# Optimization experiments

Hardware: AMD Instinct MI355X
Metric: run time of the kernel (lower is better)

Reference implementation:

```python
import jax, jax.numpy as jnp
import numpy as np
import math

B, S, D, H = 16, 1024, 768, 12
Dh = D // H  # 64


def setup_inputs() -> dict:
    key = jax.random.key(0)
    ks = jax.random.split(key, 9)
    scale = 1.0 / math.sqrt(D)
    X = jax.random.normal(ks[0], (B, S, D), dtype=jnp.float32)
    # Per-head Q/K/V projections stacked along head dim: [H, D, Dh]
    Wq = jax.random.normal(ks[1], (H, D, Dh), dtype=jnp.float32) * scale
    Wk = jax.random.normal(ks[2], (H, D, Dh), dtype=jnp.float32) * scale
    Wv = jax.random.normal(ks[3], (H, D, Dh), dtype=jnp.float32) * scale
    bq = jax.random.normal(ks[4], (H, Dh), dtype=jnp.float32) * scale
    bk = jax.random.normal(ks[5], (H, Dh), dtype=jnp.float32) * scale
    bv = jax.random.normal(ks[6], (H, Dh), dtype=jnp.float32) * scale
    Wo = jax.random.normal(ks[7], (D, D), dtype=jnp.float32) * scale
    bo = jax.random.normal(ks[8], (D,), dtype=jnp.float32) * scale
    return {"X": X, "Wq": Wq, "bq": bq, "Wk": Wk, "bk": bk,
            "Wv": Wv, "bv": bv, "Wo": Wo, "bo": bo}


def reference(X, Wq, bq, Wk, bk, Wv, bv, Wo, bo):
    # Batched multi-head QKV projections (equivalent to the per-head Linear loop).
    Q = jnp.einsum('bsd,hde->bhse', X, Wq) + bq[None, :, None, :]
    K = jnp.einsum('bsd,hde->bhse', X, Wk) + bk[None, :, None, :]
    V = jnp.einsum('bsd,hde->bhse', X, Wv) + bv[None, :, None, :]
    scores = jnp.einsum('bhse,bhte->bhst', Q, K) / jnp.sqrt(jnp.float32(Dh))
    A = jax.nn.softmax(scores, axis=-1)            # [B,H,S,S]
    O = jnp.einsum('bhst,bhte->bhse', A, V)        # [B,H,S,Dh]
    # Concat heads along feature dim (matches torch cat order: head 0 first).
    msa = jnp.transpose(O, (0, 2, 1, 3)).reshape(B, S, D)
    return msa @ Wo + bo
```

## Files before the change

### kernel.cpp

```cpp
#include <hip/hip_runtime.h>
#include <hip/hip_bf16.h>

#define BB 16
#define SS 1024
#define DD 768
#define HH 12
#define DH 64

typedef short short8 __attribute__((ext_vector_type(8)));
typedef float f32x4 __attribute__((ext_vector_type(4)));

__device__ inline float b2f(unsigned short v) {
    union { unsigned int u; float f; } x; x.u = ((unsigned int)v) << 16; return x.f;
}
__device__ inline unsigned short f2b(float f) {
    unsigned int u = __float_as_uint(f);
    u += 0x7FFFu + ((u >> 16) & 1u);
    return (unsigned short)(u >> 16);
}
__device__ inline unsigned int pk2(float a, float b) {
    __hip_bfloat162 h = __float22bfloat162_rn(make_float2(a, b));
    return *(unsigned int*)&h;
}
__device__ __forceinline__ float fast_exp2(float x) {
#if __has_builtin(__builtin_amdgcn_exp2f)
    return __builtin_amdgcn_exp2f(x);
#else
    return exp2f(x);
#endif
}
__device__ inline void cvt8(unsigned short* dst, const float* src) {
    const float4 f0 = *(const float4*)src;
    const float4 f1 = *(const float4*)(src + 4);
    unsigned short t[8] = {f2b(f0.x), f2b(f0.y), f2b(f0.z), f2b(f0.w),
                           f2b(f1.x), f2b(f1.y), f2b(f1.z), f2b(f1.w)};
    *(uint4*)dst = *(const uint4*)t;
}
__device__ __forceinline__ void async16(const void* g, void* l) {
    __builtin_amdgcn_global_load_lds(
        (const __attribute__((address_space(1))) void*)g,
        (__attribute__((address_space(3))) void*)l, 16, 0, 0);
}

__global__ __launch_bounds__(256) void detect_kernel(const unsigned short* __restrict__ X,
                                                     int* __restrict__ flag) {
    __shared__ int s;
    if (threadIdx.x == 0) s = 0;
    __syncthreads();
    int c = 0;
    for (int i = threadIdx.x; i < 16384; i += 256) {
        unsigned short v = X[i];
        if ((v & 0x7FFFu) >= 0x7F80u) c = 1;
    }
    if (c) s = 1;
    __syncthreads();
    if (threadIdx.x == 0) flag[0] = s;
}

__global__ __launch_bounds__(256) void prep_all(
    const void* __restrict__ Xv,
    const void* __restrict__ Wqv, const void* __restrict__ bqv,
    const void* __restrict__ Wkv, const void* __restrict__ bkv,
    const void* __restrict__ Wvv, const void* __restrict__ bvv,
    const void* __restrict__ Wov, const void* __restrict__ bov,
    const int* __restrict__ flag,
    unsigned short* __restrict__ Xb, unsigned short* __restrict__ Wc,
    unsigned short* __restrict__ Wot, unsigned short* __restrict__ bc,
    float* __restrict__ bo32)
{
    __shared__ unsigned short Ls[64][72];
    const int dt = *flag;
    const int u = threadIdx.x;
    const int bx = blockIdx.x;

    if (bx < 6144) {
        size_t base = ((size_t)bx * 256 + u) * 8;
        if (dt) cvt8(Xb + base, (const float*)Xv + base);
        else    *(uint4*)(Xb + base) = *(const uint4*)((const unsigned short*)Xv + base);
        return;
    }
    if (bx < 6720) {
        const int idx = bx - 6144;
        const int kt = idx % 12;
        const int y  = idx / 12;
        const int rk = u >> 2;
        const int e0 = (u & 3) * 16;

        const void* src; size_t srcBase;
        unsigned short* dst; int drow;
        if (y < 36) {
            int z = y / 12, h = y % 12;
            src = (z == 0) ? Wqv : (z == 1) ? Wkv : Wvv;
            srcBase = ((size_t)h * DD + kt * 64 + rk) * DH;
            dst = Wc; drow = z * 768 + h * 64;
        } else {
            int nt = y - 36;
            src = Wov;
            srcBase = (size_t)(kt * 64 + rk) * DD + nt * 64;
            dst = Wot; drow = nt * 64;
        }
#pragma unroll
        for (int ii = 0; ii < 2; ++ii) {
            int e = e0 + ii * 8;
            if (dt) {
                const float* p = (const float*)src + srcBase + e;
                float4 a = *(const float4*)p, b = *(const float4*)(p + 4);
                float v[8] = {a.x, a.y, a.z, a.w, b.x, b.y, b.z, b.w};
#pragma unroll
                for (int j = 0; j < 8; ++j) Ls[e + j][rk] = f2b(v[j]);
            } else {
                union { uint4 v; unsigned short s[8]; } t;
                t.v = *(const uint4*)((const unsigned short*)src + srcBase + e);
#pragma unroll
                for (int j = 0; j < 8; ++j) Ls[e + j][rk] = t.s[j];
            }
        }
        __syncthreads();
        const int e = u >> 2, q = u & 3;
#pragma unroll
        for (int ii = 0; ii < 2; ++ii) {
            int kk = q * 16 + ii * 8;
            *(uint4*)(dst + (size_t)(drow + e) * DD + kt * 64 + kk) = *(const uint4*)(&Ls[e][kk]);
        }
        return;
    }
    for (int n = u; n < 2304; n += 256) {
        int z = n / 768, i = n % 768;
        const void* b = (z == 0) ? bqv : (z == 1) ? bkv : bvv;
        bc[n] = dt ? f2b(((const float*)b)[i]) : ((const unsigned short*)b)[i];
    }
    for (int n = u; n < 768; n += 256)
        bo32[n] = dt ? ((const float*)bov)[n] : b2f(((const unsigned short*)bov)[n]);
}

__global__ __launch_bounds__(256) void qkv_gemm(
    const unsigned short* __restrict__ Xb,
    const unsigned short* __restrict__ Wc,
    const unsigned short* __restrict__ bc,
    unsigned short* __restrict__ Qb, unsigned short* __restrict__ Kb,
    unsigned short* __restrict__ Vtb)
{
    __shared__ __align__(16) unsigned short lds[17408];
    unsigned short* As = lds;
    unsigned short* Bs = lds + 128 * 64;

    const int u = threadIdx.x;
    const int lane = u & 63, w = u >> 6;
    const int ln = lane & 15, quad = lane >> 4;
    const int wm = w & 1, wn = w >> 1;

    const int nt0 = blockIdx.x;
    const int m0  = blockIdx.y << 7;
    const int n0  = nt0 << 7;
    const int z   = nt0 / 6;
    const int hpair = (nt0 % 6) * 2;

    const int rA = w * 32 + (lane >> 3);
    const int c8 = (((lane & 7) ^ (lane >> 3)) * 8);

    f32x4 acc[4][4];
#pragma unroll
    for (int i = 0; i < 4; ++i)
#pragma unroll
        for (int j = 0; j < 4; ++j) acc[i][j] = (f32x4){0.f, 0.f, 0.f, 0.f};

    const unsigned short* Ag = Xb + (size_t)(m0 + rA) * DD + c8;
    const unsigned short* Bg = Wc + (size_t)(n0 + rA) * DD + c8;
    unsigned short* lA0 = As + w * 2048;
    unsigned short* lB0 = Bs + w * 2048;

    for (int kb = 0; kb < 12; ++kb) {
        const int k0 = kb * 64;
        if (kb) __syncthreads();
#pragma unroll
        for (int j = 0; j < 4; ++j) {
            async16(Ag + (size_t)j * 8 * DD + k0, lA0 + j * 512);
            async16(Bg + (size_t)j * 8 * DD + k0, lB0 + j * 512);
        }
        __syncthreads();
#pragma unroll
        for (int kh = 0; kh < 2; ++kh) {
            const int sx = ((kh * 4 + quad) ^ (ln & 7)) * 8;
            short8 af[4], bf[4];
#pragma unroll
            for (int t = 0; t < 4; ++t) {
                af[t] = *(const short8*)(As + (wm * 64 + t * 16 + ln) * 64 + sx);
                bf[t] = *(const short8*)(Bs + (wn * 64 + t * 16 + ln) * 64 + sx);
            }
#pragma unroll
            for (int mt = 0; mt < 4; ++mt)
#pragma unroll
                for (int nt = 0; nt < 4; ++nt)
                    acc[mt][nt] = __builtin_amdgcn_mfma_f32_16x16x32_bf16(af[mt], bf[nt], acc[mt][nt], 0, 0, 0);
        }
    }

    float bias[4];
#pragma unroll
    for (int nt = 0; nt < 4; ++nt) bias[nt] = b2f(bc[n0 + wn * 64 + nt * 16 + ln]);

    const int b = m0 >> 10;
    if (z < 2) {
        unsigned short* O = (z == 0) ? Qb : Kb;
        const float sc = (z == 0) ? 0.180336880111120f : 1.0f;
        const int h = hpair + wn;
        const int sb = (m0 & 1023) + wm * 64;
#pragma unroll
        for (int mt = 0; mt < 4; ++mt)
#pragma unroll
            for (int r = 0; r < 4; ++r) {
                int s = sb + mt * 16 + quad * 4 + r;
                size_t rowo = ((size_t)(b * HH + h) * SS + s) * DH;
#pragma unroll
                for (int nt = 0; nt < 4; ++nt)
                    O[rowo + nt * 16 + ln] = f2b((acc[mt][nt][r] + bias[nt]) * sc);
            }
    } else {
        __syncthreads();
#pragma unroll
        for (int mt = 0; mt < 4; ++mt)
#pragma unroll
            for (int nt = 0; nt < 4; ++nt)
#pragma unroll
                for (int r = 0; r < 4; ++r)
                    lds[(wn * 64 + nt * 16 + ln) * 136 + wm * 64 + mt * 16 + quad * 4 + r] =
                        f2b(acc[mt][nt][r] + bias[nt]);
        __syncthreads();
        const int cc = u >> 1, half = u & 1;
        const int h = hpair + (cc >> 6), e = cc & 63;
        const int sb = (m0 & 1023) + half * 64;
        unsigned short* dst = Vtb + ((size_t)(b * HH + h) * DH + e) * SS + sb;
        const unsigned short* srcp = lds + cc * 136 + half * 64;
#pragma unroll
        for (int i = 0; i < 8; ++i)
            *(uint4*)(dst + i * 8) = *(const uint4*)(srcp + i * 8);
    }
}

__global__ __launch_bounds__(256, 3) void attn_kernel(
    const unsigned short* __restrict__ Kb,
    const unsigned short* __restrict__ Vtb,
    unsigned short* __restrict__ Qb)
{
    __shared__ __align__(16) unsigned short QPs[8192];
    __shared__ __align__(16) unsigned short Ks[2][4096];
    __shared__ __align__(16) unsigned short Vs[2][4096];

    const int u = threadIdx.x;
    const int flat = (blockIdx.y << 3) | blockIdx.x;
    const int swz  = (flat & 7) * 192 + (flat >> 3);
    const int s0 = (swz & 7) << 7;
    const int bh = swz >> 3;

    const int lane = u & 63, w = u >> 6;
    const int ln = lane & 15, quad = lane >> 4;

    unsigned short* Qg = Qb + ((size_t)bh * SS + s0) * DH;
    const unsigned short* Kg = Kb + (size_t)bh * SS * DH;
    const unsigned short* Vg = Vtb + (size_t)bh * DH * SS;

    const int srow = lane >> 3;
    const int cg8  = ((lane & 7) ^ srow) * 8;

    const unsigned short* kp0 = Kg + (size_t)((w * 2 + 0) * 8 + srow) * DH + cg8;
    const unsigned short* kp1 = Kg + (size_t)((w * 2 + 1) * 8 + srow) * DH + cg8;
    const unsigned short* vp0 = Vg + (size_t)((w * 2 + 0) * 8 + srow) * SS + cg8;
    const unsigned short* vp1 = Vg + (size_t)((w * 2 + 1) * 8 + srow) * SS + cg8;

#pragma unroll
    for (int j = 0; j < 4; ++j) {
        const int r0 = (w * 4 + j) * 8 + srow;
        async16(Qg + (size_t)r0 * DH + cg8, QPs + (w * 4 + j) * 512);
    }
    async16(kp0, &Ks[0][(w * 2 + 0) * 512]);
    async16(kp1, &Ks[0][(w * 2 + 1) * 512]);
    async16(vp0, &Vs[0][(w * 2 + 0) * 512]);
    async16(vp1, &Vs[0][(w * 2 + 1) * 512]);
    kp0 += 64 * DH; kp1 += 64 * DH; vp0 += 64; vp1 += 64;
    __syncthreads();

    short8 qf[2][2];
#pragma unroll
    for (int b = 0; b < 2; ++b) {
        const int rb = b * 64 + 16 * w + ln;
#pragma unroll
        for (int kh = 0; kh < 2; ++kh)
            qf[b][kh] = *(const short8*)(QPs + rb * 64 + ((kh * 4 + quad) ^ (ln & 7)) * 8);
    }

    short8 ones;
#pragma unroll
    for (int i = 0; i < 8; ++i) ones[i] = (short)0x3F80;

    f32x4 acc_o[2][4];
#pragma unroll
    for (int b = 0; b < 2; ++b)
#pragma unroll
        for (int i = 0; i < 4; ++i) acc_o[b][i] = (f32x4){0.f, 0.f, 0.f, 0.f};
    f32x4 acc_l[2];
    acc_l[0] = (f32x4){0.f, 0.f, 0.f, 0.f};
    acc_l[1] = (f32x4){0.f, 0.f, 0.f, 0.f};

    const unsigned short* kb0 = &Ks[0][0] + ln * 64 + ((quad ^ (ln & 7)) * 8);
    const unsigned short* kb1 = &Ks[0][0] + ln * 64 + (((4 + quad) ^ (ln & 7)) * 8);
    const unsigned short* vb0 = &Vs[0][0] + ln * 64 + ((quad ^ (ln & 7)) * 8);
    const unsigned short* vb1 = &Vs[0][0] + ln * 64 + (((4 + quad) ^ (ln & 7)) * 8);

    for (int kt = 0; kt < 16; ++kt) {
        const int cur = kt & 1;
        if (kt < 15) {
            unsigned short* lk = &Ks[cur ^ 1][(w * 2) * 512];
            unsigned short* lv = &Vs[cur ^ 1][(w * 2) * 512];
            async16(kp0, lk);
            async16(kp1, lk + 512);
            async16(vp0, lv);
            async16(vp1, lv + 512);
            kp0 += 64 * DH; kp1 += 64 * DH; vp0 += 64; vp1 += 64;
        }
        const int cb = cur * 4096;

        f32x4 acc_s[2][4];
#pragma unroll
        for (int nt = 0; nt < 4; ++nt) {
            short8 kf0 = *(const short8*)(kb0 + cb + nt * 1024);
            short8 kf1 = *(const short8*)(kb1 + cb + nt * 1024);
#pragma unroll
            for (int b = 0; b < 2; ++b) {
                f32x4 zz = (f32x4){0.f, 0.f, 0.f, 0.f};
                zz = __builtin_amdgcn_mfma_f32_16x16x32_bf16(kf0, qf[b][0], zz, 0, 0, 0);
                zz = __builtin_amdgcn_mfma_f32_16x16x32_bf16(kf1, qf[b][1], zz, 0, 0, 0);
                acc_s[b][nt] = zz;
            }
        }

#pragma unroll
        for (int b = 0; b < 2; ++b) {
            unsigned short* pb = QPs + (b * 64 + 16 * w + ln) * 64 + (quad & 1) * 4;
#pragma unroll
            for (int nt = 0; nt < 4; ++nt) {
                uint2 pw;
                pw.x = pk2(fast_exp2(acc_s[b][nt][0]), fast_exp2(acc_s[b][nt][1]));
                pw.y = pk2(fast_exp2(acc_s[b][nt][2]), fast_exp2(acc_s[b][nt][3]));
                const int c = (nt * 2 + (quad >> 1)) ^ (ln & 7);
                *(uint2*)(pb + c * 8) = pw;
            }
        }

        short8 pf[2][2];
#pragma unroll
        for (int b = 0; b < 2; ++b) {
            const unsigned short* pr = QPs + (b * 64 + 16 * w + ln) * 64;
            pf[b][0] = *(const short8*)(pr + ((quad ^ (ln & 7)) * 8));
            pf[b][1] = *(const short8*)(pr + (((4 + quad) ^ (ln & 7)) * 8));
            acc_l[b] = __builtin_amdgcn_mfma_f32_16x16x32_bf16(pf[b][0], ones, acc_l[b], 0, 0, 0);
            acc_l[b] = __builtin_amdgcn_mfma_f32_16x16x32_bf16(pf[b][1], ones, acc_l[b], 0, 0, 0);
        }
#pragma unroll
        for (int nt = 0; nt < 4; ++nt) {
            short8 vf0 = *(const short8*)(vb0 + cb + nt * 1024);
            short8 vf1 = *(const short8*)(vb1 + cb + nt * 1024);
#pragma unroll
            for (int b = 0; b < 2; ++b) {
                acc_o[b][nt] = __builtin_amdgcn_mfma_f32_16x16x32_bf16(pf[b][0], vf0, acc_o[b][nt], 0, 0, 0);
                acc_o[b][nt] = __builtin_amdgcn_mfma_f32_16x16x32_bf16(pf[b][1], vf1, acc_o[b][nt], 0, 0, 0);
            }
        }
        __syncthreads();
    }

#pragma unroll
    for (int b = 0; b < 2; ++b) {
        float inv[4];
#pragma unroll
        for (int r = 0; r < 4; ++r) inv[r] = 1.f / acc_l[b][r];
#pragma unroll
        for (int nt = 0; nt < 4; ++nt)
#pragma unroll
            for (int r = 0; r < 4; ++r) {
                int row = b * 64 + 16 * w + quad * 4 + r;
                Qg[row * DH + nt * 16 + ln] = f2b(acc_o[b][nt][r] * inv[r]);
            }
    }
}

__global__ __launch_bounds__(256) void oproj_gemm(
    const unsigned short* __restrict__ Ob,
    const unsigned short* __restrict__ Wot,
    const float* __restrict__ bo32,
    float* __restrict__ out)
{
    __shared__ __align__(16) unsigned short lds[128 * 128];
    unsigned short* As = lds;
    unsigned short* Bs = lds + 128 * 64;

    const int u = threadIdx.x;
    const int lane = u & 63, w = u >> 6;
    const int ln = lane & 15, quad = lane >> 4;
    const int wm = w & 1, wn = w >> 1;

    const int n0 = blockIdx.x << 7;
    const int m0 = blockIdx.y << 7;
    const int b = m0 >> 10, s0t = m0 & 1023;

    const int rA = w * 32 + (lane >> 3);
    const int c8 = (((lane & 7) ^ (lane >> 3)) * 8);

    f32x4 acc[4][4];
#pragma unroll
    for (int i = 0; i < 4; ++i)
#pragma unroll
        for (int j = 0; j < 4; ++j) acc[i][j] = (f32x4){0.f, 0.f, 0.f, 0.f};

    const unsigned short* Bg = Wot + (size_t)(n0 + rA) * DD + c8;
    unsigned short* lA0 = As + w * 2048;
    unsigned short* lB0 = Bs + w * 2048;

    for (int kb = 0; kb < 12; ++kb) {
        if (kb) __syncthreads();
        const unsigned short* Ag = Ob + ((size_t)(b * HH + kb) * SS + s0t + rA) * DH + c8;
#pragma unroll
        for (int j = 0; j < 4; ++j) {
            async16(Ag + (size_t)j * 8 * DH, lA0 + j * 512);
            async16(Bg + (size_t)j * 8 * DD + kb * 64, lB0 + j * 512);
        }
        __syncthreads();
#pragma unroll
        for (int kh = 0; kh < 2; ++kh) {
            const int sx = ((kh * 4 + quad) ^ (ln & 7)) * 8;
            short8 af[4], bf[4];
#pragma unroll
            for (int t = 0; t < 4; ++t) {
                af[t] = *(const short8*)(As + (wm * 64 + t * 16 + ln) * 64 + sx);
                bf[t] = *(const short8*)(Bs + (wn * 64 + t * 16 + ln) * 64 + sx);
            }
#pragma unroll
            for (int mt = 0; mt < 4; ++mt)
#pragma unroll
                for (int nt = 0; nt < 4; ++nt)
                    acc[mt][nt] = __builtin_amdgcn_mfma_f32_16x16x32_bf16(af[mt], bf[nt], acc[mt][nt], 0, 0, 0);
        }
    }

    float bias[4];
#pragma unroll
    for (int nt = 0; nt < 4; ++nt) bias[nt] = bo32[n0 + wn * 64 + nt * 16 + ln];
#pragma unroll
    for (int mt = 0; mt < 4; ++mt)
#pragma unroll
        for (int r = 0; r < 4; ++r) {
            int m = m0 + wm * 64 + mt * 16 + quad * 4 + r;
            float* orow = out + (size_t)m * DD + n0 + wn * 64;
#pragma unroll
            for (int nt = 0; nt < 4; ++nt)
                orow[nt * 16 + ln] = acc[mt][nt][r] + bias[nt];
        }
}

extern "C" void kernel_launch(void* const* d_in, const int* in_sizes, int n_in,
                              void* d_out, int out_size, void* d_ws, size_t ws_size,
                              hipStream_t stream)
{
    const void* X  = d_in[0];
    const void* Wq = d_in[1];
    const void* bq = d_in[2];
    const void* Wk = d_in[3];
    const void* bk = d_in[4];
    const void* Wv = d_in[5];
    const void* bv = d_in[6];
    const void* Wo = d_in[7];
    const void* bo = d_in[8];
    float* out = (float*)d_out;

    const size_t NE = (size_t)BB * HH * SS * DH;
    char* p = (char*)d_ws;
    int* flag = (int*)p;                 p += 256;
    unsigned short* Qb  = (unsigned short*)p;  p += NE * 2;
    unsigned short* Kb  = (unsigned short*)p;  p += NE * 2;
    unsigned short* Vtb = (unsigned short*)p;  p += NE * 2;
    unsigned short* Xb  = (unsigned short*)p;  p += (size_t)BB * SS * DD * 2;
    unsigned short* Wc  = (unsigned short*)p;  p += (size_t)3 * DD * DD * 2;
    unsigned short* Wot = (unsigned short*)p;  p += (size_t)DD * DD * 2;
    unsigned short* bcb = (unsigned short*)p;  p += 4608;
    float* bo32 = (float*)p;                   p += 3072;

    detect_kernel<<<1, 256, 0, stream>>>((const unsigned short*)X, flag);
    prep_all<<<6721, 256, 0, stream>>>(X, Wq, bq, Wk, bk, Wv, bv, Wo, bo, flag,
                                       Xb, Wc, Wot, bcb, bo32);
    qkv_gemm<<<dim3(18, 128), 256, 0, stream>>>(Xb, Wc, bcb, Qb, Kb, Vtb);
    attn_kernel<<<dim3(8, 192), 256, 0, stream>>>(Kb, Vtb, Qb);
    oproj_gemm<<<dim3(6, 128), 256, 0, stream>>>(Qb, Wot, bo32, out);
}
```

Before: 292.9 us.

## Rewrite attention inner loop with 32x32x16 MFMA and register-resident P

Switches the attention kernel from 16x16x32 to 32x32x16 bf16 MFMAs, computing S transposed so that exp'd probabilities stay in registers and are rearranged with permlane32_swap, with no round trip through LDS. The row-sum moves from an MFMA against a ones vector to a scalar VALU accumulation combined across half-waves with a shuffle. Output goes through LDS and is written with coalesced 16-byte stores, and s_setprio is raised around the MFMA blocks. It aims to cut LDS traffic and MFMA instruction count, at the cost of more accumulator registers per wave, which could hurt occupancy under the 3-blocks-per-SM bound.

```diff
diff --git a/kernel.cpp b/kernel.cpp
--- a/kernel.cpp
+++ b/kernel.cpp
@@ -9,6 +9,8 @@
 
 typedef short short8 __attribute__((ext_vector_type(8)));
 typedef float f32x4 __attribute__((ext_vector_type(4)));
+typedef float f32x16 __attribute__((ext_vector_type(16)));
+typedef unsigned int uv2 __attribute__((ext_vector_type(2)));
 
 __device__ inline float b2f(unsigned short v) {
     union { unsigned int u; float f; } x; x.u = ((unsigned int)v) << 16; return x.f;
@@ -253,7 +255,8 @@
     const int bh = swz >> 3;
 
     const int lane = u & 63, w = u >> 6;
-    const int ln = lane & 15, quad = lane >> 4;
+    const int l31 = lane & 31, hi = lane >> 5;
+    const int r7 = l31 & 7;
 
     unsigned short* Qg = Qb + ((size_t)bh * SS + s0) * DH;
     const unsigned short* Kg = Kb + (size_t)bh * SS * DH;
@@ -279,32 +282,22 @@
     kp0 += 64 * DH; kp1 += 64 * DH; vp0 += 64; vp1 += 64;
     __syncthreads();
 
-    short8 qf[2][2];
-#pragma unroll
-    for (int b = 0; b < 2; ++b) {
-        const int rb = b * 64 + 16 * w + ln;
-#pragma unroll
-        for (int kh = 0; kh < 2; ++kh)
-            qf[b][kh] = *(const short8*)(QPs + rb * 64 + ((kh * 4 + quad) ^ (ln & 7)) * 8);
-    }
-
-    short8 ones;
-#pragma unroll
-    for (int i = 0; i < 8; ++i) ones[i] = (short)0x3F80;
-
-    f32x4 acc_o[2][4];
-#pragma unroll
-    for (int b = 0; b < 2; ++b)
-#pragma unroll
-        for (int i = 0; i < 4; ++i) acc_o[b][i] = (f32x4){0.f, 0.f, 0.f, 0.f};
-    f32x4 acc_l[2];
-    acc_l[0] = (f32x4){0.f, 0.f, 0.f, 0.f};
-    acc_l[1] = (f32x4){0.f, 0.f, 0.f, 0.f};
-
-    const unsigned short* kb0 = &Ks[0][0] + ln * 64 + ((quad ^ (ln & 7)) * 8);
-    const unsigned short* kb1 = &Ks[0][0] + ln * 64 + (((4 + quad) ^ (ln & 7)) * 8);
-    const unsigned short* vb0 = &Vs[0][0] + ln * 64 + ((quad ^ (ln & 7)) * 8);
-    const unsigned short* vb1 = &Vs[0][0] + ln * 64 + (((4 + quad) ^ (ln & 7)) * 8);
+    short8 qf[4];
+    {
+        const unsigned short* qrow = QPs + (w * 32 + l31) * 64;
+#pragma unroll
+        for (int ke = 0; ke < 4; ++ke)
+            qf[ke] = *(const short8*)(qrow + (((ke * 2 + hi) ^ r7) * 8));
+    }
+
+    int off[4];
+#pragma unroll
+    for (int x = 0; x < 4; ++x) off[x] = l31 * 64 + (((x * 2 + hi) ^ r7) * 8);
+
+    f32x16 oA, oB;
+#pragma unroll
+    for (int i = 0; i < 16; ++i) { oA[i] = 0.f; oB[i] = 0.f; }
+    float lsum = 0.f;
 
     for (int kt = 0; kt < 16; ++kt) {
         const int cur = kt & 1;
@@ -317,69 +310,78 @@
             async16(vp1, lv + 512);
             kp0 += 64 * DH; kp1 += 64 * DH; vp0 += 64; vp1 += 64;
         }
-        const int cb = cur * 4096;
-
-        f32x4 acc_s[2][4];
-#pragma unroll
-        for (int nt = 0; nt < 4; ++nt) {
-            short8 kf0 = *(const short8*)(kb0 + cb + nt * 1024);
-            short8 kf1 = *(const short8*)(kb1 + cb + nt * 1024);
-#pragma unroll
-            for (int b = 0; b < 2; ++b) {
-                f32x4 zz = (f32x4){0.f, 0.f, 0.f, 0.f};
-                zz = __builtin_amdgcn_mfma_f32_16x16x32_bf16(kf0, qf[b][0], zz, 0, 0, 0);
-                zz = __builtin_amdgcn_mfma_f32_16x16x32_bf16(kf1, qf[b][1], zz, 0, 0, 0);
-                acc_s[b][nt] = zz;
-            }
-        }
-
-#pragma unroll
-        for (int b = 0; b < 2; ++b) {
-            unsigned short* pb = QPs + (b * 64 + 16 * w + ln) * 64 + (quad & 1) * 4;
-#pragma unroll
-            for (int nt = 0; nt < 4; ++nt) {
-                uint2 pw;
-                pw.x = pk2(fast_exp2(acc_s[b][nt][0]), fast_exp2(acc_s[b][nt][1]));
-                pw.y = pk2(fast_exp2(acc_s[b][nt][2]), fast_exp2(acc_s[b][nt][3]));
-                const int c = (nt * 2 + (quad >> 1)) ^ (ln & 7);
-                *(uint2*)(pb + c * 8) = pw;
-            }
-        }
-
-        short8 pf[2][2];
-#pragma unroll
-        for (int b = 0; b < 2; ++b) {
-            const unsigned short* pr = QPs + (b * 64 + 16 * w + ln) * 64;
-            pf[b][0] = *(const short8*)(pr + ((quad ^ (ln & 7)) * 8));
-            pf[b][1] = *(const short8*)(pr + (((4 + quad) ^ (ln & 7)) * 8));
-            acc_l[b] = __builtin_amdgcn_mfma_f32_16x16x32_bf16(pf[b][0], ones, acc_l[b], 0, 0, 0);
-            acc_l[b] = __builtin_amdgcn_mfma_f32_16x16x32_bf16(pf[b][1], ones, acc_l[b], 0, 0, 0);
-        }
-#pragma unroll
-        for (int nt = 0; nt < 4; ++nt) {
-            short8 vf0 = *(const short8*)(vb0 + cb + nt * 1024);
-            short8 vf1 = *(const short8*)(vb1 + cb + nt * 1024);
-#pragma unroll
-            for (int b = 0; b < 2; ++b) {
-                acc_o[b][nt] = __builtin_amdgcn_mfma_f32_16x16x32_bf16(pf[b][0], vf0, acc_o[b][nt], 0, 0, 0);
-                acc_o[b][nt] = __builtin_amdgcn_mfma_f32_16x16x32_bf16(pf[b][1], vf1, acc_o[b][nt], 0, 0, 0);
-            }
-        }
-        __syncthreads();
-    }
-
-#pragma unroll
-    for (int b = 0; b < 2; ++b) {
-        float inv[4];
-#pragma unroll
-        for (int r = 0; r < 4; ++r) inv[r] = 1.f / acc_l[b][r];
-#pragma unroll
-        for (int nt = 0; nt < 4; ++nt)
-#pragma unroll
-            for (int r = 0; r < 4; ++r) {
-                int row = b * 64 + 16 * w + quad * 4 + r;
-                Qg[row * DH + nt * 16 + ln] = f2b(acc_o[b][nt][r] * inv[r]);
-            }
+        const unsigned short* kc = Ks[cur];
+        const unsigned short* vc = Vs[cur];
+
+        f32x16 sA, sB;
+#pragma unroll
+        for (int i = 0; i < 16; ++i) { sA[i] = 0.f; sB[i] = 0.f; }
+        __builtin_amdgcn_s_setprio(1);
+#pragma unroll
+        for (int ke = 0; ke < 4; ++ke) {
+            short8 kf0 = *(const short8*)(kc + off[ke]);
+            short8 kf1 = *(const short8*)(kc + off[ke] + 2048);
+            sA = __builtin_amdgcn_mfma_f32_32x32x16_bf16(kf0, qf[ke], sA, 0, 0, 0);
+            sB = __builtin_amdgcn_mfma_f32_32x32x16_bf16(kf1, qf[ke], sB, 0, 0, 0);
+        }
+        __builtin_amdgcn_s_setprio(0);
+
+        unsigned int W0[8], W1[8];
+#pragma unroll
+        for (int i = 0; i < 8; ++i) {
+            float a0 = fast_exp2(sA[2 * i]), b0 = fast_exp2(sA[2 * i + 1]);
+            float a1 = fast_exp2(sB[2 * i]), b1 = fast_exp2(sB[2 * i + 1]);
+            lsum += (a0 + b0) + (a1 + b1);
+            W0[i] = pk2(a0, b0);
+            W1[i] = pk2(a1, b1);
+        }
+
+        __builtin_amdgcn_s_setprio(1);
+#define PV_STEP(Wt, ks) {                                                              \
+        union { unsigned int wv[4]; short8 s; } pu;                                    \
+        { uv2 rr = __builtin_amdgcn_permlane32_swap(Wt[4 * ((ks) & 1) + 0],            \
+                                                    Wt[4 * ((ks) & 1) + 2], false, false); \
+          pu.wv[0] = rr.x; pu.wv[2] = rr.y; }                                          \
+        { uv2 rr = __builtin_amdgcn_permlane32_swap(Wt[4 * ((ks) & 1) + 1],            \
+                                                    Wt[4 * ((ks) & 1) + 3], false, false); \
+          pu.wv[1] = rr.x; pu.wv[3] = rr.y; }                                          \
+        short8 vf0 = *(const short8*)(vc + off[(ks)]);                                 \
+        short8 vf1 = *(const short8*)(vc + off[(ks)] + 2048);                          \
+        oA = __builtin_amdgcn_mfma_f32_32x32x16_bf16(vf0, pu.s, oA, 0, 0, 0);          \
+        oB = __builtin_amdgcn_mfma_f32_32x32x16_bf16(vf1, pu.s, oB, 0, 0, 0); }
+        PV_STEP(W0, 0)
+        PV_STEP(W0, 1)
+        PV_STEP(W1, 2)
+        PV_STEP(W1, 3)
+#undef PV_STEP
+        __builtin_amdgcn_s_setprio(0);
+
+        __syncthreads();
+    }
+
+    float oth = __shfl(lsum, lane ^ 32, 64);
+    const float linv = 1.f / (lsum + oth);
+
+    unsigned short* Ob = QPs + w * 2048;
+#define OSTORE(oc, et) {                                                   \
+        _Pragma("unroll")                                                  \
+        for (int rg = 0; rg < 4; ++rg) {                                   \
+            uv2 wv;                                                        \
+            wv.x = pk2(oc[rg * 4 + 0] * linv, oc[rg * 4 + 1] * linv);      \
+            wv.y = pk2(oc[rg * 4 + 2] * linv, oc[rg * 4 + 3] * linv);      \
+            *(uv2*)(Ob + l31 * 64 + ((((et) * 4 + rg) ^ r7) * 8) + hi * 4) = wv; \
+        } }
+    OSTORE(oA, 0)
+    OSTORE(oB, 1)
+#undef OSTORE
+
+    const int rr2 = lane >> 1, q16 = lane & 1, rs = rr2 & 7;
+    const unsigned short* orow = QPs + w * 2048 + rr2 * 64;
+    unsigned short* gout = Qg + (size_t)(w * 32 + rr2) * DH;
+#pragma unroll
+    for (int i = 0; i < 4; ++i) {
+        const int g = q16 * 4 + i;
+        *(uint4*)(gout + g * 8) = *(const uint4*)(orow + ((g ^ rs) * 8));
     }
 }
 
```

Result: slower. 301.1 us (+2.8%).
